# Kernel tuning notes

Measured on AMD Instinct MI355X. Metric: run time of the kernel, lower is better.

Reference implementation:

```python
import jax, jax.numpy as jnp
import numpy as np

L = 16          # num transformer layers
D = 1024        # d_model
H = 16          # num heads
HD = 64         # head dim
LDIM = 512      # latent dim
TC = 512        # text conditioning length
PAST = 1024     # kv cache past length
FF = 4096       # ffn hidden
FH = 2048       # flow net hidden
MAX_PERIOD = 10000.0


def _ln(x, w, b, eps=1e-5):
    mu = jnp.mean(x, axis=-1, keepdims=True)
    var = jnp.mean((x - mu) ** 2, axis=-1, keepdims=True)
    return (x - mu) * jax.lax.rsqrt(var + eps) * w + b


def setup_inputs() -> dict:
    key = jax.random.key(0)
    ks = jax.random.split(key, 13)
    n = lambda k, s: jax.random.normal(k, s, dtype=jnp.float32)
    inp = {
        'text_embeddings': n(ks[0], (1, TC, D)),
        'prev_latent': n(ks[1], (1, 1, LDIM)),
        'kv_cache': n(ks[2], (L, 2, 1, PAST, H, HD)),
        'cache_len': PAST,
        'noise': n(ks[3], (1, LDIM)),
        'bos_emb': n(ks[4], (LDIM,)),
        'W_in': n(ks[5], (LDIM, D)) * 0.02, 'b_in': jnp.zeros((D,), jnp.float32),
        'ln1_w': jnp.ones((L, D), jnp.float32), 'ln1_b': jnp.zeros((L, D), jnp.float32),
        'Wqkv': n(ks[6], (L, D, 3 * D)) * 0.02, 'bqkv': jnp.zeros((L, 3 * D), jnp.float32),
        'Wo': n(ks[7], (L, D, D)) * 0.02, 'bo': jnp.zeros((L, D), jnp.float32),
        'ln2_w': jnp.ones((L, D), jnp.float32), 'ln2_b': jnp.zeros((L, D), jnp.float32),
        'W1': n(ks[8], (L, D, FF)) * 0.02, 'b1': jnp.zeros((L, FF), jnp.float32),
        'W2': n(ks[9], (L, FF, D)) * 0.02, 'b2': jnp.zeros((L, D), jnp.float32),
        'on_w': jnp.ones((D,), jnp.float32), 'on_b': jnp.zeros((D,), jnp.float32),
        'W_eos': n(ks[10], (D, 1)) * 0.02, 'b_eos': jnp.zeros((1,), jnp.float32),
        'Wf1': n(ks[11], (D + 2 + LDIM, FH)) * 0.02, 'bf1': jnp.zeros((FH,), jnp.float32),
        'Wf2': n(ks[12], (FH, LDIM)) * 0.02, 'bf2': jnp.zeros((LDIM,), jnp.float32),
    }
    return inp


def reference(text_embeddings, prev_latent, kv_cache, cache_len, noise, bos_emb,
              W_in, b_in, ln1_w, ln1_b, Wqkv, bqkv, Wo, bo, ln2_w, ln2_b,
              W1, b1, W2, b2, on_w, on_b, W_eos, b_eos, Wf1, bf1, Wf2, bf2):
    B = prev_latent.shape[0]
    prev = jnp.where(jnp.isnan(prev_latent), bos_emb[None, None, :], prev_latent)
    x = jnp.concatenate([text_embeddings, prev @ W_in + b_in], axis=1)  # [B,T,D]
    T = x.shape[1]
    Tkv = kv_cache.shape[3] + T

    # RoPE angles, shared across layers (offset = cache_len)
    half = HD // 2
    freqs = jnp.exp(jnp.arange(half, dtype=jnp.float32) * (-np.log(MAX_PERIOD) * 2.0 / HD))
    ts = jnp.arange(T, dtype=jnp.float32) + jnp.asarray(cache_len, jnp.float32)
    ang = ts[:, None] * freqs[None, :]               # [T, half]
    cos = jnp.cos(ang)[None, :, None, :]             # [1,T,1,half]
    sin = jnp.sin(ang)[None, :, None, :]

    # causal mask: new token q can see all past + itself
    mask = jnp.arange(Tkv)[None, :] <= (Tkv - T + jnp.arange(T)[:, None])  # [T,Tkv]
    scale = 1.0 / np.sqrt(HD)

    def rot(t):
        tr = t.reshape(B, T, H, half, 2)
        r, i = tr[..., 0], tr[..., 1]
        return jnp.stack([r * cos - i * sin, r * sin + i * cos], axis=-1).reshape(B, T, H, HD)

    def layer_fn(xc, p):
        l1w, l1b, wqkv, bq, wo, bo_, l2w, l2b, w1, b1_, w2, b2_, kv = p
        h = _ln(xc, l1w, l1b)
        qkv = (h @ wqkv + bq).reshape(B, T, 3, H, HD)
        q, k, v = qkv[:, :, 0], qkv[:, :, 1], qkv[:, :, 2]
        q, k = rot(q), rot(k)
        q = q.transpose(0, 2, 1, 3)                  # [B,H,T,HD]
        k = k.transpose(0, 2, 1, 3)
        v = v.transpose(0, 2, 1, 3)
        pk = kv[0].transpose(0, 2, 1, 3)             # [B,H,past,HD]
        pv = kv[1].transpose(0, 2, 1, 3)
        fk = jnp.concatenate([pk, k], axis=2)        # [B,H,Tkv,HD]
        fv = jnp.concatenate([pv, v], axis=2)
        scores = jnp.einsum('bhqd,bhkd->bhqk', q, fk) * scale
        scores = jnp.where(mask[None, None], scores, -1e30)
        attn = jax.nn.softmax(scores, axis=-1)
        o = jnp.einsum('bhqk,bhkd->bhqd', attn, fv).transpose(0, 2, 1, 3).reshape(B, T, D)
        xc = xc + o @ wo + bo_
        h2 = _ln(xc, l2w, l2b)
        xc = xc + jax.nn.gelu(h2 @ w1 + b1_, approximate=False) @ w2 + b2_
        new_kv = jnp.stack([fk.transpose(0, 2, 1, 3), fv.transpose(0, 2, 1, 3)])
        return xc, new_kv

    xs = (ln1_w, ln1_b, Wqkv, bqkv, Wo, bo, ln2_w, ln2_b, W1, b1, W2, b2, kv_cache)
    x, new_kv_cache = jax.lax.scan(layer_fn, x, xs)

    x = _ln(x.astype(jnp.float32), on_w, on_b)
    t_out = x[:, -1, :]                              # [B,D]
    is_eos = (t_out @ W_eos + b_eos) > -4.0
    s_time = jnp.zeros((B, 1), noise.dtype)
    t_time = jnp.ones((B, 1), noise.dtype)
    f_in = jnp.concatenate([t_out, s_time, t_time, noise], axis=-1)
    flow_dir = jax.nn.gelu(f_in @ Wf1 + bf1, approximate=False) @ Wf2 + bf2
    next_latent = noise + flow_dir
    new_cache_len = cache_len + T
    return next_latent, is_eos, new_kv_cache, new_cache_len
```

## Files before the change

### kernel.cpp

```cpp
#include <hip/hip_runtime.h>
#include <math.h>

#define KV_LS_STRIDE 1573888
#define KV_OUT_OFF 513
#define CLEN_OUT_IDX 50364929
#define VTP 1600
#define KVL 1638400

typedef __attribute__((ext_vector_type(8))) short short8;
typedef __attribute__((ext_vector_type(4))) short short4v;
typedef __attribute__((ext_vector_type(4))) float f32x4;

static __device__ __forceinline__ float gelu_f(float v){
  return 0.5f * v * (1.0f + erff(v * 0.70710678118654752f));
}
static __device__ __forceinline__ unsigned short f2b(float f){
  unsigned int u = __float_as_uint(f);
  u += 0x7fffu + ((u>>16)&1u);
  return (unsigned short)(u>>16);
}
__device__ __forceinline__ void gload16(const void* g, void* l){
  __builtin_amdgcn_global_load_lds((const __attribute__((address_space(1))) void*)g,
                                   (__attribute__((address_space(3))) void*)l, 16, 0, 0);
}

__global__ __launch_bounds__(256) void copy_text_k(const float4* __restrict__ t,
                                                   float4* __restrict__ x){
  int i = blockIdx.x*256 + threadIdx.x;
  x[i] = t[i];
}

__global__ __launch_bounds__(256) void build512_k(const float* __restrict__ prev,
    const float* __restrict__ bos, const float* __restrict__ Win,
    const float* __restrict__ bin, float* __restrict__ x){
  __shared__ float red[16][17];
  int t = threadIdx.x;
  int n = blockIdx.x*16 + (t&15), ks = t>>4;
  float s = 0.f;
  for (int k=ks*32; k<ks*32+32; ++k){
    float p = prev[k];
    if (p != p) p = bos[k];
    s += p * Win[(size_t)k*1024 + n];
  }
  red[ks][t&15] = s;
  __syncthreads();
  if (t < 16){
    float acc = bin[blockIdx.x*16 + t];
    #pragma unroll
    for (int j=0;j<16;++j) acc += red[j][t];
    x[(size_t)512*1024 + blockIdx.x*16 + t] = acc;
  }
}

__global__ __launch_bounds__(256) void rope_tab_k(float* __restrict__ cost,
    float* __restrict__ sint, const int* __restrict__ clen){
  int i = blockIdx.x*256 + threadIdx.x;
  if (i >= 513*32) return;
  int t = i >> 5, j = i & 31;
  float freq = expf((float)j * (-0.28782313662425572f));
  float ang = (float)(t + clen[0]) * freq;
  cost[i] = cosf(ang);
  sint[i] = sinf(ang);
}

template<int BF16OUT>
__global__ __launch_bounds__(256) void ln_k(const float* __restrict__ x,
    const float* __restrict__ w, const float* __restrict__ b,
    float* __restrict__ outf, unsigned short* __restrict__ outh, int rows){
  int row = blockIdx.x; if (row >= rows) return;
  const float* xr = x + (size_t)row*1024;
  int tid = threadIdx.x;
  float4 v = *(const float4*)(xr + tid*4);
  float s  = v.x+v.y+v.z+v.w;
  float ss = v.x*v.x+v.y*v.y+v.z*v.z+v.w*v.w;
  for (int o=32;o;o>>=1){ s += __shfl_down(s,o); ss += __shfl_down(ss,o); }
  __shared__ float red[8];
  int wid = tid>>6;
  if ((tid&63)==0){ red[wid]=s; red[4+wid]=ss; }
  __syncthreads();
  if (tid==0){
    float ts = red[0]+red[1]+red[2]+red[3];
    float tss= red[4]+red[5]+red[6]+red[7];
    float mu = ts*(1.0f/1024.0f);
    float var= tss*(1.0f/1024.0f) - mu*mu;
    red[0]=mu; red[1]=rsqrtf(var + 1e-5f);
  }
  __syncthreads();
  float mu = red[0], rs = red[1];
  float4 wv = *(const float4*)(w + tid*4);
  float4 bv = *(const float4*)(b + tid*4);
  float4 o4;
  o4.x = (v.x-mu)*rs*wv.x + bv.x;
  o4.y = (v.y-mu)*rs*wv.y + bv.y;
  o4.z = (v.z-mu)*rs*wv.z + bv.z;
  o4.w = (v.w-mu)*rs*wv.w + bv.w;
  if (BF16OUT){
    uint2 u;
    u.x = (unsigned)f2b(o4.x) | ((unsigned)f2b(o4.y)<<16);
    u.y = (unsigned)f2b(o4.z) | ((unsigned)f2b(o4.w)<<16);
    *(uint2*)(outh + (size_t)row*1024 + tid*4) = u;
  } else {
    *(float4*)(outf + (size_t)row*1024 + tid*4) = o4;
  }
}

__global__ __launch_bounds__(256) void wtrans_k(const float* __restrict__ W,
    unsigned short* __restrict__ Wt, int K, int N){
  __shared__ float s[64][68];
  int l = blockIdx.z;
  W  += (size_t)l*K*N;
  Wt += (size_t)l*N*K;
  int t = threadIdx.x;
  int n0 = blockIdx.x*64, k0 = blockIdx.y*64;
  int r = t>>4, c4 = (t&15)<<2;
  #pragma unroll
  for (int p=0;p<4;++p){
    float4 v = *(const float4*)(W + (size_t)(k0 + r + p*16)*N + n0 + c4);
    *(float4*)&s[r + p*16][c4] = v;
  }
  __syncthreads();
  int n = t>>2, ks = t&3;
  unsigned short tmp[16];
  #pragma unroll
  for (int j=0;j<16;++j) tmp[j] = f2b(s[ks*16 + j][n]);
  size_t ob = (size_t)(n0+n)*K + k0 + ks*16;
  uint4 lo, hi;
  lo.x = tmp[0] | ((unsigned)tmp[1]<<16);  lo.y = tmp[2] | ((unsigned)tmp[3]<<16);
  lo.z = tmp[4] | ((unsigned)tmp[5]<<16);  lo.w = tmp[6] | ((unsigned)tmp[7]<<16);
  hi.x = tmp[8] | ((unsigned)tmp[9]<<16);  hi.y = tmp[10]| ((unsigned)tmp[11]<<16);
  hi.z = tmp[12]| ((unsigned)tmp[13]<<16); hi.w = tmp[14]| ((unsigned)tmp[15]<<16);
  *(uint4*)(Wt + ob)     = lo;
  *(uint4*)(Wt + ob + 8) = hi;
}

__global__ __launch_bounds__(256) void mgemm_k(const unsigned short* __restrict__ A,
    const unsigned short* __restrict__ Bt, float* __restrict__ P,
    int M, int N, int K, int kc){
  __shared__ unsigned short Alds[128*32];
  __shared__ unsigned short Blds[128*32];
  int tid = threadIdx.x;
  int w = tid>>6, l = tid&63;
  int m0 = blockIdx.y*128, n0 = blockIdx.x*128;
  int k0 = blockIdx.z*kc, k1 = k0+kc;
  f32x4 acc[4][4];
  #pragma unroll
  for (int i=0;i<4;++i)
    #pragma unroll
    for (int j=0;j<4;++j) acc[i][j] = (f32x4){0.f,0.f,0.f,0.f};
  const unsigned short* ga  = A  + (size_t)(m0 + w*32 + (l>>2))*K + (l&3)*8;
  const unsigned short* gbp = Bt + (size_t)(n0 + w*32 + (l>>2))*K + (l&3)*8;
  unsigned short* la = &Alds[(w*32)*32];
  unsigned short* lb = &Blds[(w*32)*32];
  int wr = w>>1, wc = w&1, lr = l&15, lg = l>>4;
  for (int k=k0; k<k1; k+=32){
    gload16(ga + k,                 &la[0]);
    gload16(ga + (size_t)16*K + k,  &la[16*32]);
    gload16(gbp + k,                &lb[0]);
    gload16(gbp + (size_t)16*K + k, &lb[16*32]);
    __syncthreads();
    short8 af[4], bfr[4];
    #pragma unroll
    for (int mi=0;mi<4;++mi)
      af[mi] = *(const short8*)&Alds[(wr*64 + mi*16 + lr)*32 + lg*8];
    #pragma unroll
    for (int ni=0;ni<4;++ni)
      bfr[ni] = *(const short8*)&Blds[(wc*64 + ni*16 + lr)*32 + lg*8];
    #pragma unroll
    for (int mi=0;mi<4;++mi)
      #pragma unroll
      for (int ni=0;ni<4;++ni)
        acc[mi][ni] = __builtin_amdgcn_mfma_f32_16x16x32_bf16(af[mi], bfr[ni], acc[mi][ni], 0, 0, 0);
    __syncthreads();
  }
  float* Pz = P + (size_t)blockIdx.z*M*N;
  #pragma unroll
  for (int mi=0;mi<4;++mi){
    int rb = m0 + wr*64 + mi*16 + lg*4;
    #pragma unroll
    for (int ni=0;ni<4;++ni){
      int col = n0 + wc*64 + ni*16 + lr;
      #pragma unroll
      for (int r=0;r<4;++r){
        int row = rb + r;
        if (row < M) Pz[(size_t)row*N + col] = acc[mi][ni][r];
      }
    }
  }
}

template<int KS, int MODE>
__global__ __launch_bounds__(256) void reduce_k(const float* __restrict__ P,
    const float* __restrict__ bias, float* __restrict__ outf,
    unsigned short* __restrict__ outh, int M, int N){
  int i = blockIdx.x*256 + threadIdx.x;
  int total = (M*N)>>2;
  if (i >= total) return;
  int col4 = (i % (N>>2))<<2;
  const float4* p4 = (const float4*)P;
  float4 s = p4[i];
  #pragma unroll
  for (int z=1; z<KS; ++z){
    float4 t = p4[i + (size_t)z*total];
    s.x+=t.x; s.y+=t.y; s.z+=t.z; s.w+=t.w;
  }
  float4 bv = *(const float4*)(bias + col4);
  s.x+=bv.x; s.y+=bv.y; s.z+=bv.z; s.w+=bv.w;
  if constexpr (MODE==0){
    ((float4*)outf)[i] = s;
  } else {
    uint2 u;
    u.x = (unsigned)f2b(gelu_f(s.x)) | ((unsigned)f2b(gelu_f(s.y))<<16);
    u.y = (unsigned)f2b(gelu_f(s.z)) | ((unsigned)f2b(gelu_f(s.w))<<16);
    ((uint2*)outh)[i] = u;
  }
}

template<int KS, int DOLN>
__global__ __launch_bounds__(256) void reduce_ln_k(const float* __restrict__ P,
    const float* __restrict__ bias, float* __restrict__ x,
    const float* __restrict__ lnw, const float* __restrict__ lnb,
    unsigned short* __restrict__ outh){
  const int M = 513;
  int row = blockIdx.x;
  int tid = threadIdx.x;
  int c4 = tid<<2;
  float4 sv = *(const float4*)(P + (size_t)row*1024 + c4);
  #pragma unroll
  for (int z=1; z<KS; ++z){
    float4 t = *(const float4*)(P + (size_t)z*M*1024 + (size_t)row*1024 + c4);
    sv.x+=t.x; sv.y+=t.y; sv.z+=t.z; sv.w+=t.w;
  }
  float4 bv = *(const float4*)(bias + c4);
  float4 xv = *(const float4*)(x + (size_t)row*1024 + c4);
  xv.x += sv.x+bv.x; xv.y += sv.y+bv.y; xv.z += sv.z+bv.z; xv.w += sv.w+bv.w;
  *(float4*)(x + (size_t)row*1024 + c4) = xv;
  if constexpr (DOLN){
    float s  = xv.x+xv.y+xv.z+xv.w;
    float ss = xv.x*xv.x+xv.y*xv.y+xv.z*xv.z+xv.w*xv.w;
    for (int o=32;o;o>>=1){ s += __shfl_down(s,o); ss += __shfl_down(ss,o); }
    __shared__ float red[8];
    int wid = tid>>6;
    if ((tid&63)==0){ red[wid]=s; red[4+wid]=ss; }
    __syncthreads();
    if (tid==0){
      float ts = red[0]+red[1]+red[2]+red[3];
      float tss= red[4]+red[5]+red[6]+red[7];
      float mu = ts*(1.0f/1024.0f);
      float var= tss*(1.0f/1024.0f) - mu*mu;
      red[0]=mu; red[1]=rsqrtf(var + 1e-5f);
    }
    __syncthreads();
    float mu = red[0], rs = red[1];
    float4 wv = *(const float4*)(lnw + c4);
    float4 bb = *(const float4*)(lnb + c4);
    float o0 = (xv.x-mu)*rs*wv.x + bb.x;
    float o1 = (xv.y-mu)*rs*wv.y + bb.y;
    float o2 = (xv.z-mu)*rs*wv.z + bb.z;
    float o3 = (xv.w-mu)*rs*wv.w + bb.w;
    uint2 u;
    u.x = (unsigned)f2b(o0) | ((unsigned)f2b(o1)<<16);
    u.y = (unsigned)f2b(o2) | ((unsigned)f2b(o3)<<16);
    *(uint2*)(outh + (size_t)row*1024 + c4) = u;
  }
}

__global__ __launch_bounds__(256) void past16_k(const float* __restrict__ kvin,
    unsigned short* __restrict__ kb, unsigned short* __restrict__ vt,
    float* __restrict__ kvout){
  __shared__ float s[64][68];
  int l = blockIdx.z;
  int hh = blockIdx.x, t0 = blockIdx.y*64;
  const float* kvK = kvin + (size_t)l*2097152;
  const float* kvV = kvK + 1048576;
  unsigned short* kbL = kb + (size_t)l*KVL;
  unsigned short* vtL = vt + (size_t)l*KVL;
  float* kl = kvout + (size_t)(2*l)  *KV_LS_STRIDE;
  float* vl = kvout + (size_t)(2*l+1)*KV_LS_STRIDE;
  int tid = threadIdx.x;
  int row = tid>>4, c4 = (tid&15)<<2;
  #pragma unroll
  for (int p=0;p<4;++p){
    int rr = row + p*16;
    size_t off = (size_t)(t0+rr)*1024 + hh*64 + c4;
    float4 v = *(const float4*)(kvK + off);
    uint2 u;
    u.x = (unsigned)f2b(v.x) | ((unsigned)f2b(v.y)<<16);
    u.y = (unsigned)f2b(v.z) | ((unsigned)f2b(v.w)<<16);
    *(uint2*)(kbL + off) = u;
    kl[off]=v.x; kl[off+1]=v.y; kl[off+2]=v.z; kl[off+3]=v.w;
    float4 w = *(const float4*)(kvV + off);
    *(float4*)&s[rr][c4] = w;
    vl[off]=w.x; vl[off+1]=w.y; vl[off+2]=w.z; vl[off+3]=w.w;
  }
  __syncthreads();
  int n = tid>>2, ks = tid&3;
  unsigned short tmp[16];
  #pragma unroll
  for (int j=0;j<16;++j) tmp[j] = f2b(s[ks*16+j][n]);
  size_t ob = (size_t)(hh*64+n)*VTP + t0 + ks*16;
  uint4 lo, hi;
  lo.x = tmp[0] | ((unsigned)tmp[1]<<16);  lo.y = tmp[2] | ((unsigned)tmp[3]<<16);
  lo.z = tmp[4] | ((unsigned)tmp[5]<<16);  lo.w = tmp[6] | ((unsigned)tmp[7]<<16);
  hi.x = tmp[8] | ((unsigned)tmp[9]<<16);  hi.y = tmp[10]| ((unsigned)tmp[11]<<16);
  hi.z = tmp[12]| ((unsigned)tmp[13]<<16); hi.w = tmp[14]| ((unsigned)tmp[15]<<16);
  *(uint4*)(vtL + ob)     = lo;
  *(uint4*)(vtL + ob + 8) = hi;
}

__global__ __launch_bounds__(256) void qkv_post_k(const float* __restrict__ P,
    const float* __restrict__ bias, const float* __restrict__ cost,
    const float* __restrict__ sint, unsigned short* __restrict__ qb16,
    unsigned short* __restrict__ kb16, unsigned short* __restrict__ vt,
    float* __restrict__ kl, float* __restrict__ vl){
  __shared__ float s[64][68];
  const int M=513, N=3072;
  int hh = blockIdx.x, t0 = blockIdx.y*64;
  int tid = threadIdx.x;
  int row = tid>>4, c4 = (tid&15)<<2;
  #pragma unroll
  for (int p=0;p<4;++p){
    int rr = row + p*16;
    int t = t0 + rr;
    float4 vv = make_float4(0.f,0.f,0.f,0.f);
    if (t < M){
      const float* p0 = P + (size_t)t*N + hh*64 + c4;
      const float* p1 = p0 + (size_t)M*N;
      float4 a, b;
      a = *(const float4*)p0; b = *(const float4*)p1;
      float4 qv = make_float4(a.x+b.x, a.y+b.y, a.z+b.z, a.w+b.w);
      a = *(const float4*)(p0+1024); b = *(const float4*)(p1+1024);
      float4 kv = make_float4(a.x+b.x, a.y+b.y, a.z+b.z, a.w+b.w);
      a = *(const float4*)(p0+2048); b = *(const float4*)(p1+2048);
      vv = make_float4(a.x+b.x, a.y+b.y, a.z+b.z, a.w+b.w);
      float4 bq = *(const float4*)(bias + hh*64 + c4);
      float4 bk = *(const float4*)(bias + 1024 + hh*64 + c4);
      float4 bvv= *(const float4*)(bias + 2048 + hh*64 + c4);
      qv.x+=bq.x; qv.y+=bq.y; qv.z+=bq.z; qv.w+=bq.w;
      kv.x+=bk.x; kv.y+=bk.y; kv.z+=bk.z; kv.w+=bk.w;
      vv.x+=bvv.x; vv.y+=bvv.y; vv.z+=bvv.z; vv.w+=bvv.w;
      int jj = c4>>1;
      float c0 = cost[(t<<5)+jj],   s0 = sint[(t<<5)+jj];
      float c1 = cost[(t<<5)+jj+1], s1 = sint[(t<<5)+jj+1];
      float q0 = qv.x*c0 - qv.y*s0, q1 = qv.x*s0 + qv.y*c0;
      float q2 = qv.z*c1 - qv.w*s1, q3 = qv.z*s1 + qv.w*c1;
      float k0 = kv.x*c0 - kv.y*s0, k1 = kv.x*s0 + kv.y*c0;
      float k2 = kv.z*c1 - kv.w*s1, k3 = kv.z*s1 + kv.w*c1;
      uint2 uq;
      uq.x = (unsigned)f2b(q0) | ((unsigned)f2b(q1)<<16);
      uq.y = (unsigned)f2b(q2) | ((unsigned)f2b(q3)<<16);
      *(uint2*)(qb16 + (size_t)t*1024 + hh*64 + c4) = uq;
      uint2 uk;
      uk.x = (unsigned)f2b(k0) | ((unsigned)f2b(k1)<<16);
      uk.y = (unsigned)f2b(k2) | ((unsigned)f2b(k3)<<16);
      size_t ko = (size_t)(1024+t)*1024 + hh*64 + c4;
      *(uint2*)(kb16 + ko) = uk;
      kl[ko]=k0; kl[ko+1]=k1; kl[ko+2]=k2; kl[ko+3]=k3;
      vl[ko]=vv.x; vl[ko+1]=vv.y; vl[ko+2]=vv.z; vl[ko+3]=vv.w;
    }
    *(float4*)&s[rr][c4] = vv;
  }
  __syncthreads();
  int n = tid>>2, ks = tid&3;
  unsigned short tmp[16];
  #pragma unroll
  for (int j=0;j<16;++j) tmp[j] = f2b(s[ks*16+j][n]);
  size_t ob = (size_t)(hh*64+n)*VTP + 1024 + t0 + ks*16;
  uint4 lo, hi;
  lo.x = tmp[0] | ((unsigned)tmp[1]<<16);  lo.y = tmp[2] | ((unsigned)tmp[3]<<16);
  lo.z = tmp[4] | ((unsigned)tmp[5]<<16);  lo.w = tmp[6] | ((unsigned)tmp[7]<<16);
  hi.x = tmp[8] | ((unsigned)tmp[9]<<16);  hi.y = tmp[10]| ((unsigned)tmp[11]<<16);
  hi.z = tmp[12]| ((unsigned)tmp[13]<<16); hi.w = tmp[14]| ((unsigned)tmp[15]<<16);
  *(uint4*)(vt + ob)     = lo;
  *(uint4*)(vt + ob + 8) = hi;
}

static __device__ __forceinline__ f32x4 mfma32(short8 a, short8 b, f32x4 c){
  return __builtin_amdgcn_mfma_f32_16x16x32_bf16(a, b, c, 0, 0, 0);
}

__global__ __launch_bounds__(128) void attn_k(const unsigned short* __restrict__ qb,
    const unsigned short* __restrict__ kb, const unsigned short* __restrict__ vt,
    float* __restrict__ Oc, float* __restrict__ ml){
  const int T=513, Tkv=1537, past=1024;
  int hh = blockIdx.x, bt = blockIdx.y, ch = blockIdx.z;
  int wv = threadIdx.x >> 6, l = threadIdx.x & 63;
  int g = l >> 4, lr = l & 15;
  int q0 = bt*32 + wv*16;
  int gq = q0 + lr;
  const unsigned short* qp = qb + (size_t)gq*1024 + hh*64 + g*8;
  short8 qf0 = *(const short8*)qp;
  short8 qf1 = *(const short8*)(qp+32);
  f32x4 acc_o[4];
  #pragma unroll
  for (int i=0;i<4;++i) acc_o[i] = (f32x4){0.f,0.f,0.f,0.f};
  float m_run = -1e30f, l_run = 0.f;
  int kend_w = past + q0 + 16; if (kend_w > Tkv) kend_w = Tkv;
  int kstart = ch*384;
  int kend = (ch==3) ? kend_w : ((ch+1)*384 < kend_w ? (ch+1)*384 : kend_w);
  const float scale = 0.125f;
  for (int kt0 = kstart; kt0 < kend; kt0 += 64){
    float p[16];
    #pragma unroll
    for (int st=0; st<4; ++st){
      const unsigned short* kp = kb + (size_t)(kt0+st*16+lr)*1024 + hh*64 + g*8;
      short8 kf0 = *(const short8*)kp;
      short8 kf1 = *(const short8*)(kp+32);
      f32x4 s4 = (f32x4){0.f,0.f,0.f,0.f};
      s4 = mfma32(kf0, qf0, s4);
      s4 = mfma32(kf1, qf1, s4);
      #pragma unroll
      for (int r=0;r<4;++r) p[st*4+r] = s4[r]*scale;
    }
    if (kt0 + 63 > past + q0 + 15 || kt0 + 63 >= Tkv){
      #pragma unroll
      for (int st=0; st<4; ++st)
        #pragma unroll
        for (int r=0;r<4;++r){
          int kt = kt0 + st*16 + g*4 + r;
          if (kt > past + gq || kt >= Tkv) p[st*4+r] = -1e30f;
        }
    }
    float tmax = p[0];
    #pragma unroll
    for (int i=1;i<16;++i) tmax = fmaxf(tmax, p[i]);
    tmax = fmaxf(tmax, __shfl_xor(tmax,16));
    tmax = fmaxf(tmax, __shfl_xor(tmax,32));
    float m_new = fmaxf(m_run, tmax);
    float sc = __expf(m_run - m_new);
    float psum = 0.f;
    #pragma unroll
    for (int i=0;i<16;++i){ p[i] = __expf(p[i] - m_new); psum += p[i]; }
    psum += __shfl_xor(psum,16); psum += __shfl_xor(psum,32);
    l_run = l_run*sc + psum;
    m_run = m_new;
    #pragma unroll
    for (int db=0;db<4;++db){
      acc_o[db][0]*=sc; acc_o[db][1]*=sc; acc_o[db][2]*=sc; acc_o[db][3]*=sc;
    }
    short8 pf[4];
    #pragma unroll
    for (int st=0; st<4; ++st){
      union { short8 s8; unsigned int u[4]; } pu;
      pu.u[0] = (unsigned)f2b(p[st*4+0]) | ((unsigned)f2b(p[st*4+1])<<16);
      pu.u[1] = (unsigned)f2b(p[st*4+2]) | ((unsigned)f2b(p[st*4+3])<<16);
      pu.u[2] = 0; pu.u[3] = 0;
      pf[st] = pu.s8;
    }
    #pragma unroll
    for (int st=0; st<4; ++st){
      #pragma unroll
      for (int db=0; db<4; ++db){
        const unsigned short* vp = vt + (size_t)(hh*64 + db*16 + lr)*VTP + kt0 + st*16 + g*4;
        short4v v4 = *(const short4v*)vp;
        short8 va = (short8){v4[0],v4[1],v4[2],v4[3],0,0,0,0};
        acc_o[db] = mfma32(va, pf[st], acc_o[db]);
      }
    }
  }
  if (gq < T){
    size_t ob = ((size_t)(ch*16+hh)*544 + gq)*64;
    #pragma unroll
    for (int db=0;db<4;++db)
      *(float4*)(Oc + ob + db*16 + g*4) = make_float4(acc_o[db][0],acc_o[db][1],acc_o[db][2],acc_o[db][3]);
    if (g==0){
      size_t mo = ((size_t)(ch*16+hh)*544 + gq)*2;
      ml[mo] = m_run; ml[mo+1] = l_run;
    }
  }
}

__global__ __launch_bounds__(256) void attn_comb_k(const float* __restrict__ Oc,
    const float* __restrict__ ml, unsigned short* __restrict__ obb){
  int qg = blockIdx.x;
  int t = threadIdx.x;
  int hh = t>>4, d4 = (t&15)<<2;
  float m[4], lv[4];
  float mm = -1e30f;
  #pragma unroll
  for (int c=0;c<4;++c){
    size_t mo = ((size_t)(c*16+hh)*544 + qg)*2;
    m[c]=ml[mo]; lv[c]=ml[mo+1];
    mm = fmaxf(mm, m[c]);
  }
  float w[4], denom = 0.f;
  #pragma unroll
  for (int c=0;c<4;++c){ w[c] = __expf(m[c]-mm); denom += lv[c]*w[c]; }
  float inv = 1.0f/denom;
  float r0=0.f,r1=0.f,r2=0.f,r3=0.f;
  #pragma unroll
  for (int c=0;c<4;++c){
    float4 o = *(const float4*)(Oc + (((size_t)(c*16+hh)*544+qg)*64 + d4));
    r0 += o.x*w[c]; r1 += o.y*w[c]; r2 += o.z*w[c]; r3 += o.w*w[c];
  }
  r0*=inv; r1*=inv; r2*=inv; r3*=inv;
  uint2 u;
  u.x = (unsigned)f2b(r0) | ((unsigned)f2b(r1)<<16);
  u.y = (unsigned)f2b(r2) | ((unsigned)f2b(r3)<<16);
  *(uint2*)(obb + (size_t)qg*1024 + hh*64 + d4) = u;
}

__global__ __launch_bounds__(256) void eos_tail_k(const float* __restrict__ tout,
    const float* __restrict__ Weos, const float* __restrict__ beos,
    const int* __restrict__ clen, float* __restrict__ out){
  int tid = threadIdx.x;
  float s = 0.f;
  for (int i=tid;i<1024;i+=256) s += tout[i]*Weos[i];
  for (int o=32;o;o>>=1) s += __shfl_down(s,o);
  __shared__ float red[4];
  if ((tid&63)==0) red[tid>>6] = s;
  __syncthreads();
  if (tid==0){
    float v = red[0]+red[1]+red[2]+red[3] + beos[0];
    out[512] = (v > -4.0f) ? 1.0f : 0.0f;
    out[CLEN_OUT_IDX] = (float)(clen[0] + 513);
  }
}

__global__ __launch_bounds__(256) void flow1_k(const float* __restrict__ tout,
    const float* __restrict__ noise, const float* __restrict__ Wf1,
    const float* __restrict__ bf1, float* __restrict__ fh){
  __shared__ float red[16][17];
  int t = threadIdx.x;
  int n = blockIdx.x*16 + (t&15), ks = t>>4;
  float s = 0.f;
  for (int k=ks*96; k<ks*96+96; ++k){
    float in = (k < 1024) ? tout[k] : noise[k-1024];
    size_t krow = (k < 1024) ? (size_t)k : (size_t)(k+2);
    s += in * Wf1[krow*2048 + n];
  }
  red[ks][t&15] = s;
  __syncthreads();
  if (t < 16){
    int nn = blockIdx.x*16 + t;
    float acc = bf1[nn] + Wf1[(size_t)1025*2048 + nn];
    #pragma unroll
    for (int j=0;j<16;++j) acc += red[j][t];
    fh[nn] = gelu_f(acc);
  }
}

__global__ __launch_bounds__(256) void flow2_k(const float* __restrict__ fh,
    const float* __restrict__ noise, const float* __restrict__ Wf2,
    const float* __restrict__ bf2, float* __restrict__ out){
  __shared__ float red[16][17];
  int t = threadIdx.x;
  int n = blockIdx.x*16 + (t&15), ks = t>>4;
  float s = 0.f;
  for (int k=ks*128; k<ks*128+128; ++k) s += fh[k]*Wf2[(size_t)k*512 + n];
  red[ks][t&15] = s;
  __syncthreads();
  if (t < 16){
    int nn = blockIdx.x*16 + t;
    float acc = bf2[nn];
    #pragma unroll
    for (int j=0;j<16;++j) acc += red[j][t];
    out[nn] = noise[nn] + acc;
  }
}

extern "C" void kernel_launch(void* const* d_in, const int* in_sizes, int n_in,
                              void* d_out, int out_size, void* d_ws, size_t ws_size,
                              hipStream_t stream) {
  const float* text  = (const float*)d_in[0];
  const float* prevl = (const float*)d_in[1];
  const float* kvin  = (const float*)d_in[2];
  const int*   clen  = (const int*)  d_in[3];
  const float* noise = (const float*)d_in[4];
  const float* bos   = (const float*)d_in[5];
  const float* Win   = (const float*)d_in[6];
  const float* bin   = (const float*)d_in[7];
  const float* ln1w  = (const float*)d_in[8];
  const float* ln1b  = (const float*)d_in[9];
  const float* Wqkv  = (const float*)d_in[10];
  const float* bqkv  = (const float*)d_in[11];
  const float* Wo    = (const float*)d_in[12];
  const float* bo    = (const float*)d_in[13];
  const float* ln2w  = (const float*)d_in[14];
  const float* ln2b  = (const float*)d_in[15];
  const float* W1    = (const float*)d_in[16];
  const float* b1    = (const float*)d_in[17];
  const float* W2    = (const float*)d_in[18];
  const float* b2    = (const float*)d_in[19];
  const float* onw   = (const float*)d_in[20];
  const float* onb   = (const float*)d_in[21];
  const float* Weos  = (const float*)d_in[22];
  const float* beos  = (const float*)d_in[23];
  const float* Wf1   = (const float*)d_in[24];
  const float* bf1   = (const float*)d_in[25];
  const float* Wf2   = (const float*)d_in[26];
  const float* bf2   = (const float*)d_in[27];

  float* out   = (float*)d_out;
  float* kvout = out + KV_OUT_OFF;
  float* ws = (float*)d_ws;
  float* x    = ws;
  float* Pbuf = x    + 525312;
  float* Oc   = Pbuf + 4202496;
  float* mlb  = Oc   + 2228224;
  float* cost = mlb  + 69632;
  float* sint = cost + 16416;
  float* tout = sint + 16416;
  float* fh   = tout + 1024;
  unsigned short* hb   = (unsigned short*)(fh + 2048);
  unsigned short* gb   = hb   + 655360;
  unsigned short* obb  = gb   + 2621440;
  unsigned short* qb16 = obb  + 655360;
  unsigned short* kb16 = qb16 + 557056;
  unsigned short* vt16 = kb16 + (size_t)16*KVL;
  unsigned short* qkvT = vt16 + (size_t)16*KVL;
  unsigned short* woT  = qkvT + (size_t)16*3145728;
  unsigned short* w1T  = woT  + (size_t)16*1048576;
  unsigned short* w2T  = w1T  + (size_t)16*4194304;

  past16_k<<<dim3(16,16,16),256,0,stream>>>(kvin, kb16, vt16, kvout);
  wtrans_k<<<dim3(48,16,16),256,0,stream>>>(Wqkv, qkvT, 1024, 3072);
  wtrans_k<<<dim3(16,16,16),256,0,stream>>>(Wo,   woT,  1024, 1024);
  wtrans_k<<<dim3(64,16,16),256,0,stream>>>(W1,   w1T,  1024, 4096);
  wtrans_k<<<dim3(16,64,16),256,0,stream>>>(W2,   w2T,  4096, 1024);
  copy_text_k<<<512,256,0,stream>>>((const float4*)text, (float4*)x);
  build512_k<<<64,256,0,stream>>>(prevl, bos, Win, bin, x);
  rope_tab_k<<<65,256,0,stream>>>(cost, sint, clen);
  ln_k<1><<<513,256,0,stream>>>(x, ln1w, ln1b, nullptr, hb, 513);

  for (int l=0; l<16; ++l){
    float* kl = kvout + (size_t)(2*l)  *KV_LS_STRIDE;
    float* vl = kvout + (size_t)(2*l+1)*KV_LS_STRIDE;
    unsigned short* kbL = kb16 + (size_t)l*KVL;
    unsigned short* vtL = vt16 + (size_t)l*KVL;
    mgemm_k<<<dim3(24,5,2),256,0,stream>>>(hb, qkvT+(size_t)l*3145728, Pbuf, 513, 3072, 1024, 512);
    qkv_post_k<<<dim3(16,9),256,0,stream>>>(Pbuf, bqkv+(size_t)l*3072, cost, sint,
        qb16, kbL, vtL, kl, vl);
    attn_k<<<dim3(16,17,4),128,0,stream>>>(qb16, kbL, vtL, Oc, mlb);
    attn_comb_k<<<513,256,0,stream>>>(Oc, mlb, obb);
    mgemm_k<<<dim3(8,5,4),256,0,stream>>>(obb, woT+(size_t)l*1048576, Pbuf, 513, 1024, 1024, 256);
    reduce_ln_k<4,1><<<513,256,0,stream>>>(Pbuf, bo+(size_t)l*1024, x,
        ln2w+(size_t)l*1024, ln2b+(size_t)l*1024, hb);
    mgemm_k<<<dim3(32,5,2),256,0,stream>>>(hb, w1T+(size_t)l*4194304, Pbuf, 513, 4096, 1024, 512);
    reduce_k<2,2><<<2052,256,0,stream>>>(Pbuf, b1+(size_t)l*4096, nullptr, gb, 513, 4096);
    mgemm_k<<<dim3(8,5,4),256,0,stream>>>(gb, w2T+(size_t)l*4194304, Pbuf, 513, 1024, 4096, 1024);
    if (l < 15)
      reduce_ln_k<4,1><<<513,256,0,stream>>>(Pbuf, b2+(size_t)l*1024, x,
          ln1w+(size_t)(l+1)*1024, ln1b+(size_t)(l+1)*1024, hb);
    else
      reduce_ln_k<4,0><<<513,256,0,stream>>>(Pbuf, b2+(size_t)l*1024, x,
          nullptr, nullptr, nullptr);
  }

  ln_k<0><<<1,256,0,stream>>>(x + (size_t)512*1024, onw, onb, tout, nullptr, 1);
  eos_tail_k<<<1,256,0,stream>>>(tout, Weos, beos, clen, out);
  flow1_k<<<128,256,0,stream>>>(tout, noise, Wf1, bf1, fh);
  flow2_k<<<32,256,0,stream>>>(fh, noise, Wf2, bf2, out);
}
```

Baseline: 2.763 ms.

## Fuse bias and GELU epilogues into GEMM, drop split-K for QKV and FFN1

The QKV and FFN-up GEMMs no longer use split-K. They now apply the bias, and for FFN-up also GELU with the bf16 conversion, inside the GEMM epilogue. This removes the separate reduce kernel and the write and re-read of split-K partials. The attention softmax scale is folded into Q during the post-processing pass. The trade-off is fewer blocks in flight for these GEMMs (120 and 160 blocks instead of twice that), which lowers parallelism on the GPU's many CUs, and the epilogue now does scalar bf16 stores.

After: 3.239 ms. +17.2%, slower.

```diff
diff --git a/kernel.cpp b/kernel.cpp
--- a/kernel.cpp
+++ b/kernel.cpp
@@ -133,8 +133,10 @@
   *(uint4*)(Wt + ob + 8) = hi;
 }
 
+template<int MODE>
 __global__ __launch_bounds__(256) void mgemm_k(const unsigned short* __restrict__ A,
     const unsigned short* __restrict__ Bt, float* __restrict__ P,
+    const float* __restrict__ bias, unsigned short* __restrict__ outh,
     int M, int N, int K, int kc){
   __shared__ unsigned short Alds[128*32];
   __shared__ unsigned short Blds[128*32];
@@ -179,39 +181,21 @@
     #pragma unroll
     for (int ni=0;ni<4;++ni){
       int col = n0 + wc*64 + ni*16 + lr;
+      float bcol = (MODE!=0) ? bias[col] : 0.f;
       #pragma unroll
       for (int r=0;r<4;++r){
         int row = rb + r;
-        if (row < M) Pz[(size_t)row*N + col] = acc[mi][ni][r];
+        if (row < M){
+          if constexpr (MODE==0){
+            Pz[(size_t)row*N + col] = acc[mi][ni][r];
+          } else if constexpr (MODE==1){
+            P[(size_t)row*N + col] = acc[mi][ni][r] + bcol;
+          } else {
+            outh[(size_t)row*N + col] = f2b(gelu_f(acc[mi][ni][r] + bcol));
+          }
+        }
       }
     }
-  }
-}
-
-template<int KS, int MODE>
-__global__ __launch_bounds__(256) void reduce_k(const float* __restrict__ P,
-    const float* __restrict__ bias, float* __restrict__ outf,
-    unsigned short* __restrict__ outh, int M, int N){
-  int i = blockIdx.x*256 + threadIdx.x;
-  int total = (M*N)>>2;
-  if (i >= total) return;
-  int col4 = (i % (N>>2))<<2;
-  const float4* p4 = (const float4*)P;
-  float4 s = p4[i];
-  #pragma unroll
-  for (int z=1; z<KS; ++z){
-    float4 t = p4[i + (size_t)z*total];
-    s.x+=t.x; s.y+=t.y; s.z+=t.z; s.w+=t.w;
-  }
-  float4 bv = *(const float4*)(bias + col4);
-  s.x+=bv.x; s.y+=bv.y; s.z+=bv.z; s.w+=bv.w;
-  if constexpr (MODE==0){
-    ((float4*)outf)[i] = s;
-  } else {
-    uint2 u;
-    u.x = (unsigned)f2b(gelu_f(s.x)) | ((unsigned)f2b(gelu_f(s.y))<<16);
-    u.y = (unsigned)f2b(gelu_f(s.z)) | ((unsigned)f2b(gelu_f(s.w))<<16);
-    ((uint2*)outh)[i] = u;
   }
 }
 
@@ -308,10 +292,9 @@
 }
 
 __global__ __launch_bounds__(256) void qkv_post_k(const float* __restrict__ P,
-    const float* __restrict__ bias, const float* __restrict__ cost,
-    const float* __restrict__ sint, unsigned short* __restrict__ qb16,
-    unsigned short* __restrict__ kb16, unsigned short* __restrict__ vt,
-    float* __restrict__ kl, float* __restrict__ vl){
+    const float* __restrict__ cost, const float* __restrict__ sint,
+    unsigned short* __restrict__ qb16, unsigned short* __restrict__ kb16,
+    unsigned short* __restrict__ vt, float* __restrict__ kl, float* __restrict__ vl){
   __shared__ float s[64][68];
   const int M=513, N=3072;
   int hh = blockIdx.x, t0 = blockIdx.y*64;
@@ -324,25 +307,14 @@
     float4 vv = make_float4(0.f,0.f,0.f,0.f);
     if (t < M){
       const float* p0 = P + (size_t)t*N + hh*64 + c4;
-      const float* p1 = p0 + (size_t)M*N;
-      float4 a, b;
-      a = *(const float4*)p0; b = *(const float4*)p1;
-      float4 qv = make_float4(a.x+b.x, a.y+b.y, a.z+b.z, a.w+b.w);
-      a = *(const float4*)(p0+1024); b = *(const float4*)(p1+1024);
-      float4 kv = make_float4(a.x+b.x, a.y+b.y, a.z+b.z, a.w+b.w);
-      a = *(const float4*)(p0+2048); b = *(const float4*)(p1+2048);
-      vv = make_float4(a.x+b.x, a.y+b.y, a.z+b.z, a.w+b.w);
-      float4 bq = *(const float4*)(bias + hh*64 + c4);
-      float4 bk = *(const float4*)(bias + 1024 + hh*64 + c4);
-      float4 bvv= *(const float4*)(bias + 2048 + hh*64 + c4);
-      qv.x+=bq.x; qv.y+=bq.y; qv.z+=bq.z; qv.w+=bq.w;
-      kv.x+=bk.x; kv.y+=bk.y; kv.z+=bk.z; kv.w+=bk.w;
-      vv.x+=bvv.x; vv.y+=bvv.y; vv.z+=bvv.z; vv.w+=bvv.w;
+      float4 qv = *(const float4*)p0;
+      float4 kv = *(const float4*)(p0+1024);
+      vv        = *(const float4*)(p0+2048);
       int jj = c4>>1;
       float c0 = cost[(t<<5)+jj],   s0 = sint[(t<<5)+jj];
       float c1 = cost[(t<<5)+jj+1], s1 = sint[(t<<5)+jj+1];
-      float q0 = qv.x*c0 - qv.y*s0, q1 = qv.x*s0 + qv.y*c0;
-      float q2 = qv.z*c1 - qv.w*s1, q3 = qv.z*s1 + qv.w*c1;
+      float q0 = (qv.x*c0 - qv.y*s0)*0.125f, q1 = (qv.x*s0 + qv.y*c0)*0.125f;
+      float q2 = (qv.z*c1 - qv.w*s1)*0.125f, q3 = (qv.z*s1 + qv.w*c1)*0.125f;
       float k0 = kv.x*c0 - kv.y*s0, k1 = kv.x*s0 + kv.y*c0;
       float k2 = kv.z*c1 - kv.w*s1, k3 = kv.z*s1 + kv.w*c1;
       uint2 uq;
@@ -397,7 +369,6 @@
   int kend_w = past + q0 + 16; if (kend_w > Tkv) kend_w = Tkv;
   int kstart = ch*384;
   int kend = (ch==3) ? kend_w : ((ch+1)*384 < kend_w ? (ch+1)*384 : kend_w);
-  const float scale = 0.125f;
   for (int kt0 = kstart; kt0 < kend; kt0 += 64){
     float p[16];
     #pragma unroll
@@ -409,7 +380,7 @@
       s4 = mfma32(kf0, qf0, s4);
       s4 = mfma32(kf1, qf1, s4);
       #pragma unroll
-      for (int r=0;r<4;++r) p[st*4+r] = s4[r]*scale;
+      for (int r=0;r<4;++r) p[st*4+r] = s4[r];
     }
     if (kt0 + 63 > past + q0 + 15 || kt0 + 63 >= Tkv){
       #pragma unroll
@@ -627,17 +598,19 @@
     float* vl = kvout + (size_t)(2*l+1)*KV_LS_STRIDE;
     unsigned short* kbL = kb16 + (size_t)l*KVL;
     unsigned short* vtL = vt16 + (size_t)l*KVL;
-    mgemm_k<<<dim3(24,5,2),256,0,stream>>>(hb, qkvT+(size_t)l*3145728, Pbuf, 513, 3072, 1024, 512);
-    qkv_post_k<<<dim3(16,9),256,0,stream>>>(Pbuf, bqkv+(size_t)l*3072, cost, sint,
-        qb16, kbL, vtL, kl, vl);
+    mgemm_k<1><<<dim3(24,5,1),256,0,stream>>>(hb, qkvT+(size_t)l*3145728, Pbuf,
+        bqkv+(size_t)l*3072, nullptr, 513, 3072, 1024, 1024);
+    qkv_post_k<<<dim3(16,9),256,0,stream>>>(Pbuf, cost, sint, qb16, kbL, vtL, kl, vl);
     attn_k<<<dim3(16,17,4),128,0,stream>>>(qb16, kbL, vtL, Oc, mlb);
     attn_comb_k<<<513,256,0,stream>>>(Oc, mlb, obb);
-    mgemm_k<<<dim3(8,5,4),256,0,stream>>>(obb, woT+(size_t)l*1048576, Pbuf, 513, 1024, 1024, 256);
+    mgemm_k<0><<<dim3(8,5,4),256,0,stream>>>(obb, woT+(size_t)l*1048576, Pbuf,
+        nullptr, nullptr, 513, 1024, 1024, 256);
     reduce_ln_k<4,1><<<513,256,0,stream>>>(Pbuf, bo+(size_t)l*1024, x,
         ln2w+(size_t)l*1024, ln2b+(size_t)l*1024, hb);
-    mgemm_k<<<dim3(32,5,2),256,0,stream>>>(hb, w1T+(size_t)l*4194304, Pbuf, 513, 4096, 1024, 512);
-    reduce_k<2,2><<<2052,256,0,stream>>>(Pbuf, b1+(size_t)l*4096, nullptr, gb, 513, 4096);
-    mgemm_k<<<dim3(8,5,4),256,0,stream>>>(gb, w2T+(size_t)l*4194304, Pbuf, 513, 1024, 4096, 1024);
+    mgemm_k<2><<<dim3(32,5,1),256,0,stream>>>(hb, w1T+(size_t)l*4194304, Pbuf,
+        b1+(size_t)l*4096, gb, 513, 4096, 1024, 1024);
+    mgemm_k<0><<<dim3(8,5,4),256,0,stream>>>(gb, w2T+(size_t)l*4194304, Pbuf,
+        nullptr, nullptr, 513, 1024, 4096, 1024);
     if (l < 15)
       reduce_ln_k<4,1><<<513,256,0,stream>>>(Pbuf, b2+(size_t)l*1024, x,
           ln1w+(size_t)(l+1)*1024, ln1b+(size_t)(l+1)*1024, hb);
```
